# Kernel optimization log

Hardware: AMD Instinct MI355X
Metric: run time of the kernel (lower is better)

Reference implementation:

```python
import jax, jax.numpy as jnp
import numpy as np

EPS = 1e-6
SCALE_END = 1.0


def _rms_norm(x, w):
    # x: [B, L, H, D], w: [D]
    var = jnp.mean(jnp.square(x), axis=-1, keepdims=True)
    return x * jax.lax.rsqrt(var + EPS) * w


def _apply_rope(x, freqs):
    # x: [B, L, H, D]; freqs: [L, D//2] rotation angles.
    # Interleaved pair rotation: (x0, x1) -> (x0*cos - x1*sin, x0*sin + x1*cos)
    B, L, H, D = x.shape
    xr = x.reshape(B, L, H, D // 2, 2)
    x0, x1 = xr[..., 0], xr[..., 1]
    cos = jnp.cos(freqs)[None, :, None, :]  # [1, L, 1, D//2]
    sin = jnp.sin(freqs)[None, :, None, :]
    o0 = x0 * cos - x1 * sin
    o1 = x0 * sin + x1 * cos
    return jnp.stack([o0, o1], axis=-1).reshape(B, L, H, D)


def setup_inputs() -> dict:
    key = jax.random.key(0)
    ks = jax.random.split(key, 6)
    B, Lq, Lk, H, D = 1, 4096, 1024, 24, 128
    hidden = H * D
    query = jax.random.normal(ks[0], (B, Lq, H, D), dtype=jnp.float32)
    ref_latent = jax.random.normal(ks[1], (B, Lk, hidden), dtype=jnp.float32)
    ref_freqs = jax.random.uniform(ks[2], (Lk, D // 2), dtype=jnp.float32)
    Wk = jax.random.normal(ks[3], (hidden, hidden), dtype=jnp.float32) * (hidden ** -0.5)
    Wv = jax.random.normal(ks[4], (hidden, hidden), dtype=jnp.float32) * (hidden ** -0.5)
    rms_w = jnp.ones((D,), dtype=jnp.float32)
    return {"query": query, "ref_latent": ref_latent, "ref_freqs": ref_freqs,
            "Wk": Wk, "Wv": Wv, "rms_w": rms_w}


def reference(query, ref_latent, ref_freqs, Wk, Wv, rms_w):
    B, Lq, H, D = query.shape
    # K/V projections (nn.Linear: y = x @ W.T)
    ref_k = jnp.einsum('ble,he->blh', ref_latent, Wk).reshape(B, -1, H, D)
    ref_v = jnp.einsum('ble,he->blh', ref_latent, Wv).reshape(B, -1, H, D)
    # RMSNorm on K heads, then rotary embedding on K
    ref_k = _rms_norm(ref_k, rms_w)
    ref_k = _apply_rope(ref_k, ref_freqs)
    # Non-causal attention, softmax_scale = head_dim ** -0.5 (flash_attn layout B L H D)
    scale = D ** -0.5
    scores = jnp.einsum('bqhd,bkhd->bhqk', query, ref_k) * scale
    probs = jax.nn.softmax(scores, axis=-1)
    attn = jnp.einsum('bhqk,bkhd->bqhd', probs, ref_v)
    attn = attn.reshape(B, Lq, H * D)
    return SCALE_END * attn
```

## Files before the change

### kernel.cpp

```cpp
#include <hip/hip_runtime.h>
#include <hip/hip_bf16.h>

typedef __attribute__((ext_vector_type(8))) short short8;
typedef float floatx4 __attribute__((ext_vector_type(4)));
typedef float floatx16 __attribute__((ext_vector_type(16)));

#define LQ 4096
#define LK 1024
#define NH 24
#define HD 128
#define HID 3072

__device__ __forceinline__ unsigned short f2bf(float f) {
    __hip_bfloat16 h = __float2bfloat16(f);
    union { __hip_bfloat16 b; unsigned short u; } c; c.b = h;
    return c.u;
}

__device__ __forceinline__ unsigned cvtpk(float a, float b) {
    unsigned r;
    asm("v_cvt_pk_bf16_f32 %0, %1, %2" : "=v"(r) : "v"(a), "v"(b));
    return r;
}

__device__ __forceinline__ float fexp2(float x) {
    float r;
    asm("v_exp_f32 %0, %1" : "=v"(r) : "v"(x));
    return r;
}

__device__ __forceinline__ void gload16(const void* g, void* l) {
    __builtin_amdgcn_global_load_lds(
        (const __attribute__((address_space(1))) void*)g,
        (__attribute__((address_space(3))) void*)l,
        16, 0, 0);
}

__global__ void f32_to_bf16(const float* __restrict__ in, unsigned short* __restrict__ out, int n4) {
    int i = blockIdx.x * blockDim.x + threadIdx.x;
    int stride = gridDim.x * blockDim.x;
    for (; i < n4; i += stride) {
        float4 v = ((const float4*)in)[i];
        ushort4 o;
        o.x = f2bf(v.x); o.y = f2bf(v.y); o.z = f2bf(v.z); o.w = f2bf(v.w);
        ((ushort4*)out)[i] = o;
    }
}

__global__ __launch_bounds__(256) void gemm_proj(const unsigned short* __restrict__ A,
                                                 const unsigned short* __restrict__ Bw,
                                                 float* __restrict__ C,
                                                 int M, int N, int K) {
    __shared__ __align__(16) unsigned short As[2][64 * 64];
    __shared__ __align__(16) unsigned short Bs[2][128 * 64];
    const int tid = threadIdx.x;
    const int lane = tid & 63;
    const int wave = tid >> 6;
    const int wm = wave >> 1, wn = wave & 1;
    const int flat = blockIdx.x + gridDim.x * blockIdx.y;
    const int wid = (flat & 7) * 48 + (flat >> 3);
    const int bm0 = (wid & 15) * 64;
    const int bn0 = (wid >> 4) * 128;
    const int kbeg = blockIdx.z * (K >> 1);
    const int kend = kbeg + (K >> 1);
    float* Cz = C + (size_t)blockIdx.z * M * N;
    const int lr = lane & 15;
    const int lg = lane >> 4;

    floatx4 acc[2][4];
    for (int i = 0; i < 2; ++i)
        for (int j = 0; j < 4; ++j)
            acc[i][j] = (floatx4){0.f, 0.f, 0.f, 0.f};

    auto stage = [&](int b, int k0) {
        for (int p = 0; p < 2; ++p) {
            int slot = p * 256 + tid;
            int r = slot >> 3, cb = slot & 7;
            int g = cb ^ (r & 7);
            gload16(&A[(bm0 + r) * K + k0 + g * 8], &As[b][(p * 256 + wave * 64) * 8]);
        }
        for (int p = 0; p < 4; ++p) {
            int slot = p * 256 + tid;
            int r = slot >> 3, cb = slot & 7;
            int g = cb ^ (r & 7);
            gload16(&Bw[(bn0 + r) * K + k0 + g * 8], &Bs[b][(p * 256 + wave * 64) * 8]);
        }
    };

    auto compute = [&](int b) {
        for (int ks = 0; ks < 2; ++ks) {
            short8 af[2], bfr[4];
            for (int mt = 0; mt < 2; ++mt) {
                int m = wm * 32 + mt * 16 + lr;
                int sc = (ks * 4 + lg) ^ (m & 7);
                af[mt] = *(const short8*)(&As[b][m * 64 + sc * 8]);
            }
            for (int nt = 0; nt < 4; ++nt) {
                int n = wn * 64 + nt * 16 + lr;
                int sc = (ks * 4 + lg) ^ (n & 7);
                bfr[nt] = *(const short8*)(&Bs[b][n * 64 + sc * 8]);
            }
            __builtin_amdgcn_s_setprio(1);
            for (int mt = 0; mt < 2; ++mt)
                for (int nt = 0; nt < 4; ++nt)
                    acc[mt][nt] = __builtin_amdgcn_mfma_f32_16x16x32_bf16(af[mt], bfr[nt], acc[mt][nt], 0, 0, 0);
            __builtin_amdgcn_s_setprio(0);
        }
    };

    stage(0, kbeg);
    __syncthreads();
    int buf = 0;
    for (int k0 = kbeg; k0 < kend - 64; k0 += 64) {
        stage(buf ^ 1, k0 + 64);
        compute(buf);
        __syncthreads();
        buf ^= 1;
    }
    compute(buf);

    for (int mt = 0; mt < 2; ++mt)
        for (int nt = 0; nt < 4; ++nt)
            for (int rg = 0; rg < 4; ++rg) {
                int m = bm0 + wm * 32 + mt * 16 + lg * 4 + rg;
                int n = bn0 + wn * 64 + nt * 16 + lr;
                Cz[m * N + n] = acc[mt][nt][rg];
            }
}

__global__ __launch_bounds__(256) void rmsnorm_rope(const float* __restrict__ r0,
                                                    const float* __restrict__ r1,
                                                    const float* __restrict__ freqs,
                                                    const float* __restrict__ w,
                                                    unsigned short* __restrict__ Kbf) {
    int row = blockIdx.x * 2 + (threadIdx.x >> 7);
    int l = row / NH, h = row % NH;
    int d = threadIdx.x & 127;
    int idx = l * HID + h * HD + d;
    float x = r0[idx] + r1[idx];
    float ss = x * x;
    for (int off = 32; off; off >>= 1) ss += __shfl_xor(ss, off);
    __shared__ float red[4];
    int wv = threadIdx.x >> 6;
    if ((threadIdx.x & 63) == 0) red[wv] = ss;
    __syncthreads();
    int base = (threadIdx.x >> 7) * 2;
    float tot = red[base] + red[base + 1];
    float rsn = rsqrtf(tot * (1.0f / 128.0f) + 1e-6f);
    float xn = x * rsn * w[d];
    float f = freqs[l * (HD / 2) + (d >> 1)];
    float s = __sinf(f), c = __cosf(f);
    float partner = __shfl_xor(xn, 1);
    float o = (d & 1) ? (partner * s + xn * c) : (xn * c - partner * s);
    Kbf[idx] = f2bf(o);
}

__global__ __launch_bounds__(256) void transpose_v(const float* __restrict__ r0,
                                                   const float* __restrict__ r1,
                                                   unsigned short* __restrict__ Vfrag) {
    __shared__ float tile[32][65];
    const int bx = blockIdx.x;
    const int by = blockIdx.y;
    const int hd0 = bx * 64, l0 = by * 32;
    const int tx = threadIdx.x & 63;
    const int tg8 = threadIdx.x >> 6;
    for (int i = 0; i < 8; ++i) {
        int r = tg8 * 8 + i;
        int idx = (l0 + r) * HID + hd0 + tx;
        tile[r][tx] = r0[idx] + r1[idx];
    }
    __syncthreads();
    const int tg = threadIdx.x >> 6;
    const int c = tg >> 1, hi = tg & 1;
    const int hdl = threadIdx.x & 63;
    const int kloc = c * 16 + hi * 8;
    short8 v;
    for (int j = 0; j < 8; ++j)
        v[j] = (short)f2bf(tile[kloc + j][hdl]);
    const int hd = hd0 + hdl;
    const int h = hd >> 7;
    const int ntd = (hd & 127) >> 5;
    const int l31 = hd & 31;
    size_t pos = ((((size_t)(h * 32 + by) * 4 + ntd) * 2 + c) * 2 + hi) * 32 + l31;
    *(short8*)(&Vfrag[pos * 8]) = v;
}

__global__ __launch_bounds__(256, 3) void attn(const float* __restrict__ Q,
                                               const unsigned short* __restrict__ Kbf,
                                               const unsigned short* __restrict__ Vfrag,
                                               float* __restrict__ O) {
    __shared__ __align__(16) unsigned short Ks[2][32 * 128];
    __shared__ __align__(16) unsigned short Vs[2][32 * 128];
    const int tid = threadIdx.x;
    const int lane = tid & 63;
    const int wave = tid >> 6;
    const int l31 = lane & 31;
    const int hi = lane >> 5;
    const int flat = blockIdx.x + gridDim.x * blockIdx.y;
    const int wid = (flat & 7) * 96 + (flat >> 3);
    const int h = wid >> 5;
    const int q0 = (wid & 31) * 128 + wave * 32;
    const float qscale = 0.08838834764831843f * 1.44269504088896340736f;
    const float SHIFT = 32.0f;
    const int NT = LK / 32;

    short8 qf[8];
#pragma unroll
    for (int m = 0; m < 8; ++m) {
        const float* qp = &Q[(q0 + l31) * HID + h * HD + m * 16 + hi * 8];
        float4 lo = *(const float4*)(qp);
        float4 hif = *(const float4*)(qp + 4);
        short8 v;
        v[0] = (short)f2bf(lo.x * qscale);
        v[1] = (short)f2bf(lo.y * qscale);
        v[2] = (short)f2bf(lo.z * qscale);
        v[3] = (short)f2bf(lo.w * qscale);
        v[4] = (short)f2bf(hif.x * qscale);
        v[5] = (short)f2bf(hif.y * qscale);
        v[6] = (short)f2bf(hif.z * qscale);
        v[7] = (short)f2bf(hif.w * qscale);
        qf[m] = v;
    }

    floatx16 accO[4];
#pragma unroll
    for (int i = 0; i < 4; ++i)
#pragma unroll
        for (int r = 0; r < 16; ++r) accO[i][r] = 0.f;
    float psum = 0.f;

    auto stageK = [&](int b, int kt) {
        for (int i = 0; i < 2; ++i) {
            int slot = i * 256 + tid;
            int r = slot >> 4, bb = slot & 15;
            int g = bb ^ (r & 15);
            gload16(&Kbf[(kt * 32 + r) * HID + h * HD + g * 8],
                    &Ks[b][(i * 256 + wave * 64) * 8]);
        }
    };
    auto stageV = [&](int b, int kt) {
        const unsigned short* src = Vfrag + ((size_t)(h * 32 + kt) << 12);
        for (int i = 0; i < 2; ++i) {
            int slot = i * 256 + tid;
            gload16(&src[slot * 8], &Vs[b][(i * 256 + wave * 64) * 8]);
        }
    };

    auto compute = [&](int b) {
        floatx16 sa, sb;
#pragma unroll
        for (int r = 0; r < 16; ++r) { sa[r] = -SHIFT; sb[r] = 0.f; }
        __builtin_amdgcn_s_setprio(1);
#pragma unroll
        for (int m = 0; m < 4; ++m) {
            int ca = m * 2 + hi;
            int cb2 = (m + 4) * 2 + hi;
            int slota = l31 * 16 + (ca ^ (l31 & 15));
            int slotb = l31 * 16 + (cb2 ^ (l31 & 15));
            short8 kfa = *(const short8*)(&Ks[b][slota * 8]);
            short8 kfb = *(const short8*)(&Ks[b][slotb * 8]);
            sa = __builtin_amdgcn_mfma_f32_32x32x16_bf16(kfa, qf[m], sa, 0, 0, 0);
            sb = __builtin_amdgcn_mfma_f32_32x32x16_bf16(kfb, qf[m + 4], sb, 0, 0, 0);
        }
        __builtin_amdgcn_s_setprio(0);
        float e[16];
#pragma unroll
        for (int r = 0; r < 16; ++r) e[r] = fexp2(sa[r] + sb[r]);
        {
            float s01 = e[0] + e[1],   s23 = e[2] + e[3];
            float s45 = e[4] + e[5],   s67 = e[6] + e[7];
            float s89 = e[8] + e[9],   sab = e[10] + e[11];
            float scd = e[12] + e[13], sef = e[14] + e[15];
            float t0 = s01 + s23, t1 = s45 + s67, t2 = s89 + sab, t3 = scd + sef;
            psum += (t0 + t1) + (t2 + t3);
        }
        unsigned d0 = cvtpk(e[0], e[1]),   d1 = cvtpk(e[2], e[3]);
        unsigned d2 = cvtpk(e[4], e[5]),   d3 = cvtpk(e[6], e[7]);
        unsigned d4 = cvtpk(e[8], e[9]),   d5 = cvtpk(e[10], e[11]);
        unsigned d6 = cvtpk(e[12], e[13]), d7 = cvtpk(e[14], e[15]);
        asm volatile("v_permlane32_swap_b32 %0, %1" : "+v"(d0), "+v"(d2));
        asm volatile("v_permlane32_swap_b32 %0, %1" : "+v"(d1), "+v"(d3));
        asm volatile("v_permlane32_swap_b32 %0, %1" : "+v"(d4), "+v"(d6));
        asm volatile("v_permlane32_swap_b32 %0, %1" : "+v"(d5), "+v"(d7));
        union { unsigned u[4]; short8 s; } p0, p1;
        p0.u[0] = d0; p0.u[1] = d1; p0.u[2] = d2; p0.u[3] = d3;
        p1.u[0] = d4; p1.u[1] = d5; p1.u[2] = d6; p1.u[3] = d7;
        __builtin_amdgcn_s_setprio(1);
#pragma unroll
        for (int ntd = 0; ntd < 4; ++ntd) {
            int s0 = ((ntd * 2 + 0) * 2 + hi) * 32 + l31;
            int s1 = ((ntd * 2 + 1) * 2 + hi) * 32 + l31;
            short8 vf0 = *(const short8*)(&Vs[b][s0 * 8]);
            short8 vf1 = *(const short8*)(&Vs[b][s1 * 8]);
            accO[ntd] = __builtin_amdgcn_mfma_f32_32x32x16_bf16(p0.s, vf0, accO[ntd], 0, 0, 0);
            accO[ntd] = __builtin_amdgcn_mfma_f32_32x32x16_bf16(p1.s, vf1, accO[ntd], 0, 0, 0);
        }
        __builtin_amdgcn_s_setprio(0);
    };

    stageK(0, 0);
    stageV(0, 0);
    __syncthreads();
    int buf = 0;
    for (int t = 0; t < NT - 1; ++t) {
        stageK(buf ^ 1, t + 1);
        stageV(buf ^ 1, t + 1);
        compute(buf);
        __syncthreads();
        buf ^= 1;
    }
    compute(buf);

    float s = psum + __shfl_xor(psum, 32);
    float rinv = 1.0f / s;
    float ri[16];
#pragma unroll
    for (int r = 0; r < 16; ++r) {
        int row = (r & 3) + 8 * (r >> 2) + 4 * hi;
        ri[r] = __shfl(rinv, row);
    }
#pragma unroll
    for (int ntd = 0; ntd < 4; ++ntd)
#pragma unroll
        for (int r = 0; r < 16; ++r) {
            int row = (r & 3) + 8 * (r >> 2) + 4 * hi;
            O[(q0 + row) * HID + h * HD + ntd * 32 + l31] = accO[ntd][r] * ri[r];
        }
}

extern "C" void kernel_launch(void* const* d_in, const int* in_sizes, int n_in,
                              void* d_out, int out_size, void* d_ws, size_t ws_size,
                              hipStream_t stream) {
    const float* Q      = (const float*)d_in[0];
    const float* latent = (const float*)d_in[1];
    const float* freqs  = (const float*)d_in[2];
    const float* Wk     = (const float*)d_in[3];
    const float* Wv     = (const float*)d_in[4];
    const float* rmsw   = (const float*)d_in[5];
    float* out = (float*)d_out;
    char* ws = (char*)d_ws;

    unsigned short* latent_bf = (unsigned short*)(ws);
    unsigned short* Wbf       = (unsigned short*)(ws + 6291456);
    float*          raw0      = (float*)(ws + 25165824);
    float*          raw1      = (float*)(ws + 37748736);
    unsigned short* Kbf       = (unsigned short*)(ws + 50331648);
    unsigned short* Vfrag     = (unsigned short*)(ws + 56623104);

    f32_to_bf16<<<2048, 256, 0, stream>>>(latent, latent_bf, (LK * HID) / 4);
    f32_to_bf16<<<2048, 256, 0, stream>>>(Wk, Wbf, (HID * HID) / 4);

    gemm_proj<<<dim3(16, 24, 2), 256, 0, stream>>>(latent_bf, Wbf, raw0, LK, HID, HID);
    rmsnorm_rope<<<(LK * NH) / 2, 256, 0, stream>>>(raw0, raw1, freqs, rmsw, Kbf);

    f32_to_bf16<<<2048, 256, 0, stream>>>(Wv, Wbf, (HID * HID) / 4);
    gemm_proj<<<dim3(16, 24, 2), 256, 0, stream>>>(latent_bf, Wbf, raw0, LK, HID, HID);
    transpose_v<<<dim3(HID / 64, LK / 32), 256, 0, stream>>>(raw0, raw1, Vfrag);

    attn<<<dim3(LQ / 128, NH), 256, 0, stream>>>(Q, Kbf, Vfrag, out);
}
```

Measured before the change: 165.1 us.

## Triple-buffer K/V LDS staging with partial vmcnt waits

Expands the K and V shared-memory tiles from double to triple buffering and prefetches two tiles ahead. The loop now waits only until the older loads have finished (vmcnt(4)) before each barrier, so the next tile's global loads can stay in flight during compute. The aim is to hide global-load latency behind the MFMA work. The cost is more LDS per block, which may cut occupancy under launch_bounds(256,3), and correctness depends on the stage functions issuing exactly four vector memory ops per tile.

```diff
diff --git a/kernel.cpp b/kernel.cpp
--- a/kernel.cpp
+++ b/kernel.cpp
@@ -189,8 +189,8 @@
                                                const unsigned short* __restrict__ Kbf,
                                                const unsigned short* __restrict__ Vfrag,
                                                float* __restrict__ O) {
-    __shared__ __align__(16) unsigned short Ks[2][32 * 128];
-    __shared__ __align__(16) unsigned short Vs[2][32 * 128];
+    __shared__ __align__(16) unsigned short Ks[3][32 * 128];
+    __shared__ __align__(16) unsigned short Vs[3][32 * 128];
     const int tid = threadIdx.x;
     const int lane = tid & 63;
     const int wave = tid >> 6;
@@ -298,18 +298,27 @@
         __builtin_amdgcn_s_setprio(0);
     };
 
-    stageK(0, 0);
-    stageV(0, 0);
-    __syncthreads();
-    int buf = 0;
-    for (int t = 0; t < NT - 1; ++t) {
-        stageK(buf ^ 1, t + 1);
-        stageV(buf ^ 1, t + 1);
-        compute(buf);
-        __syncthreads();
-        buf ^= 1;
-    }
-    compute(buf);
+    stageK(0, 0); stageV(0, 0);
+    stageK(1, 1); stageV(1, 1);
+    asm volatile("s_waitcnt vmcnt(4)" ::: "memory");
+    __builtin_amdgcn_s_barrier();
+
+    for (int t = 0; t < NT; ++t) {
+        if (t + 2 < NT) {
+            int nb = (t + 2) % 3;
+            stageK(nb, t + 2);
+            stageV(nb, t + 2);
+            compute(t % 3);
+            asm volatile("s_waitcnt vmcnt(4)" ::: "memory");
+            __builtin_amdgcn_s_barrier();
+        } else if (t + 1 < NT) {
+            compute(t % 3);
+            asm volatile("s_waitcnt vmcnt(0)" ::: "memory");
+            __builtin_amdgcn_s_barrier();
+        } else {
+            compute(t % 3);
+        }
+    }
 
     float s = psum + __shfl_xor(psum, 32);
     float rinv = 1.0f / s;
```

Result: no change. 165.3 us (+0.1%).

## Process two key tiles per iteration with split K/V staging in attention

Applied to the files above, without the earlier changes.

The attention loop now handles two 32-key tiles per iteration: tile t and tile t+16. This halves the iteration count and gives two independent full-depth QK MFMA chains, where before one tile was split across two half-depth accumulators. K tiles stay double-buffered and are prefetched one iteration ahead. V tiles now share a single buffer that is loaded at the top of each iteration, with a barrier between the softmax and the PV stage. The goal is more instruction-level parallelism and better hiding of load latency, at the cost of more LDS per block (48KB), which may limit occupancy, and of V load latency that is only partly covered by the QK and softmax work.

```diff
diff --git a/kernel.cpp b/kernel.cpp
--- a/kernel.cpp
+++ b/kernel.cpp
@@ -189,8 +189,10 @@
                                                const unsigned short* __restrict__ Kbf,
                                                const unsigned short* __restrict__ Vfrag,
                                                float* __restrict__ O) {
-    __shared__ __align__(16) unsigned short Ks[2][32 * 128];
-    __shared__ __align__(16) unsigned short Vs[2][32 * 128];
+    __shared__ __align__(16) unsigned short KA[2][32 * 128];
+    __shared__ __align__(16) unsigned short KB[2][32 * 128];
+    __shared__ __align__(16) unsigned short VA[32 * 128];
+    __shared__ __align__(16) unsigned short VB[32 * 128];
     const int tid = threadIdx.x;
     const int lane = tid & 63;
     const int wave = tid >> 6;
@@ -202,7 +204,6 @@
     const int q0 = (wid & 31) * 128 + wave * 32;
     const float qscale = 0.08838834764831843f * 1.44269504088896340736f;
     const float SHIFT = 32.0f;
-    const int NT = LK / 32;
 
     short8 qf[8];
 #pragma unroll
@@ -229,43 +230,27 @@
         for (int r = 0; r < 16; ++r) accO[i][r] = 0.f;
     float psum = 0.f;
 
-    auto stageK = [&](int b, int kt) {
+    auto stageK = [&](unsigned short* dst, int kt) {
         for (int i = 0; i < 2; ++i) {
             int slot = i * 256 + tid;
             int r = slot >> 4, bb = slot & 15;
             int g = bb ^ (r & 15);
             gload16(&Kbf[(kt * 32 + r) * HID + h * HD + g * 8],
-                    &Ks[b][(i * 256 + wave * 64) * 8]);
-        }
-    };
-    auto stageV = [&](int b, int kt) {
+                    &dst[(i * 256 + wave * 64) * 8]);
+        }
+    };
+    auto stageV = [&](unsigned short* dst, int kt) {
         const unsigned short* src = Vfrag + ((size_t)(h * 32 + kt) << 12);
         for (int i = 0; i < 2; ++i) {
             int slot = i * 256 + tid;
-            gload16(&src[slot * 8], &Vs[b][(i * 256 + wave * 64) * 8]);
-        }
-    };
-
-    auto compute = [&](int b) {
-        floatx16 sa, sb;
-#pragma unroll
-        for (int r = 0; r < 16; ++r) { sa[r] = -SHIFT; sb[r] = 0.f; }
-        __builtin_amdgcn_s_setprio(1);
-#pragma unroll
-        for (int m = 0; m < 4; ++m) {
-            int ca = m * 2 + hi;
-            int cb2 = (m + 4) * 2 + hi;
-            int slota = l31 * 16 + (ca ^ (l31 & 15));
-            int slotb = l31 * 16 + (cb2 ^ (l31 & 15));
-            short8 kfa = *(const short8*)(&Ks[b][slota * 8]);
-            short8 kfb = *(const short8*)(&Ks[b][slotb * 8]);
-            sa = __builtin_amdgcn_mfma_f32_32x32x16_bf16(kfa, qf[m], sa, 0, 0, 0);
-            sb = __builtin_amdgcn_mfma_f32_32x32x16_bf16(kfb, qf[m + 4], sb, 0, 0, 0);
-        }
-        __builtin_amdgcn_s_setprio(0);
+            gload16(&src[slot * 8], &dst[(i * 256 + wave * 64) * 8]);
+        }
+    };
+
+    auto softmax32 = [&](floatx16 s, short8& pa, short8& pb) {
         float e[16];
 #pragma unroll
-        for (int r = 0; r < 16; ++r) e[r] = fexp2(sa[r] + sb[r]);
+        for (int r = 0; r < 16; ++r) e[r] = fexp2(s[r]);
         {
             float s01 = e[0] + e[1],   s23 = e[2] + e[3];
             float s45 = e[4] + e[5],   s67 = e[6] + e[7];
@@ -285,31 +270,55 @@
         union { unsigned u[4]; short8 s; } p0, p1;
         p0.u[0] = d0; p0.u[1] = d1; p0.u[2] = d2; p0.u[3] = d3;
         p1.u[0] = d4; p1.u[1] = d5; p1.u[2] = d6; p1.u[3] = d7;
+        pa = p0.s; pb = p1.s;
+    };
+
+    stageK(KA[0], 0);
+    stageK(KB[0], 16);
+    asm volatile("s_waitcnt vmcnt(0)" ::: "memory");
+    __builtin_amdgcn_s_barrier();
+
+    for (int t = 0; t < 16; ++t) {
+        stageV(VA, t);
+        stageV(VB, t + 16);
+        if (t < 15) {
+            stageK(KA[(t + 1) & 1], t + 1);
+            stageK(KB[(t + 1) & 1], t + 17);
+        }
+        floatx16 sA, sB;
+#pragma unroll
+        for (int r = 0; r < 16; ++r) { sA[r] = -SHIFT; sB[r] = -SHIFT; }
+        __builtin_amdgcn_s_setprio(1);
+#pragma unroll
+        for (int m = 0; m < 8; ++m) {
+            int slot = l31 * 16 + ((m * 2 + hi) ^ (l31 & 15));
+            short8 kfa = *(const short8*)(&KA[t & 1][slot * 8]);
+            short8 kfb = *(const short8*)(&KB[t & 1][slot * 8]);
+            sA = __builtin_amdgcn_mfma_f32_32x32x16_bf16(kfa, qf[m], sA, 0, 0, 0);
+            sB = __builtin_amdgcn_mfma_f32_32x32x16_bf16(kfb, qf[m], sB, 0, 0, 0);
+        }
+        __builtin_amdgcn_s_setprio(0);
+        short8 pA0, pA1, pB0, pB1;
+        softmax32(sA, pA0, pA1);
+        softmax32(sB, pB0, pB1);
+        __syncthreads();
         __builtin_amdgcn_s_setprio(1);
 #pragma unroll
         for (int ntd = 0; ntd < 4; ++ntd) {
             int s0 = ((ntd * 2 + 0) * 2 + hi) * 32 + l31;
             int s1 = ((ntd * 2 + 1) * 2 + hi) * 32 + l31;
-            short8 vf0 = *(const short8*)(&Vs[b][s0 * 8]);
-            short8 vf1 = *(const short8*)(&Vs[b][s1 * 8]);
-            accO[ntd] = __builtin_amdgcn_mfma_f32_32x32x16_bf16(p0.s, vf0, accO[ntd], 0, 0, 0);
-            accO[ntd] = __builtin_amdgcn_mfma_f32_32x32x16_bf16(p1.s, vf1, accO[ntd], 0, 0, 0);
+            short8 vA0 = *(const short8*)(&VA[s0 * 8]);
+            short8 vA1 = *(const short8*)(&VA[s1 * 8]);
+            short8 vB0 = *(const short8*)(&VB[s0 * 8]);
+            short8 vB1 = *(const short8*)(&VB[s1 * 8]);
+            accO[ntd] = __builtin_amdgcn_mfma_f32_32x32x16_bf16(pA0, vA0, accO[ntd], 0, 0, 0);
+            accO[ntd] = __builtin_amdgcn_mfma_f32_32x32x16_bf16(pA1, vA1, accO[ntd], 0, 0, 0);
+            accO[ntd] = __builtin_amdgcn_mfma_f32_32x32x16_bf16(pB0, vB0, accO[ntd], 0, 0, 0);
+            accO[ntd] = __builtin_amdgcn_mfma_f32_32x32x16_bf16(pB1, vB1, accO[ntd], 0, 0, 0);
         }
         __builtin_amdgcn_s_setprio(0);
-    };
-
-    stageK(0, 0);
-    stageV(0, 0);
-    __syncthreads();
-    int buf = 0;
-    for (int t = 0; t < NT - 1; ++t) {
-        stageK(buf ^ 1, t + 1);
-        stageV(buf ^ 1, t + 1);
-        compute(buf);
         __syncthreads();
-        buf ^= 1;
-    }
-    compute(buf);
+    }
 
     float s = psum + __shfl_xor(psum, 32);
     float rinv = 1.0f / s;
```

New measurement: 161.6 us. 2.1% less time.
